# Optimization experiments

Measured on AMD Instinct MI355X. Metric: run time of the kernel, lower is better.

The kernel has to match this reference:

```python
import jax, jax.numpy as jnp
import numpy as np

EPS_BN = 1e-5
EPS_COS = 1e-8
N, E, D = 50000, 1600000, 128
HGC, LG, NUM_CLASSES, EIN, PAE_H = 64, 4, 2, 12, 128


def setup_inputs() -> dict:
    key = jax.random.key(0)
    ks = jax.random.split(key, 16)
    kaiming = lambda k, fi, fo: jax.random.normal(k, (fi, fo), jnp.float32) * (2.0 / fi) ** 0.5
    glorot = lambda k, shape: jax.random.normal(k, shape, jnp.float32) * (2.0 / (shape[-2] + shape[-1])) ** 0.5
    inp = {}
    inp["features"] = jax.random.normal(ks[0], (N, D), jnp.float32)
    inp["edge_index"] = jax.random.randint(ks[1], (2, E), 0, N, jnp.int32)
    inp["edgenet_input"] = jax.random.normal(ks[2], (E, EIN), jnp.float32)
    # PAE parser: Linear(6,128) -> ReLU -> BN(128) -> Dropout -> Linear(128,128)
    inp["pae_w1"] = kaiming(ks[3], EIN // 2, PAE_H)
    inp["pae_b1"] = jnp.zeros((PAE_H,), jnp.float32)
    inp["pae_bn_g"] = jnp.ones((PAE_H,), jnp.float32)
    inp["pae_bn_b"] = jnp.zeros((PAE_H,), jnp.float32)
    inp["pae_bn_rm"] = jnp.zeros((PAE_H,), jnp.float32)
    inp["pae_bn_rv"] = jnp.ones((PAE_H,), jnp.float32)
    inp["pae_w2"] = kaiming(ks[4], PAE_H, PAE_H)
    inp["pae_b2"] = jnp.zeros((PAE_H,), jnp.float32)
    # ChebConv weights, K=3, bias=False: [K, in, out]
    inp["cheb_w0"] = glorot(ks[5], (3, D, HGC))
    inp["cheb_w1"] = glorot(ks[6], (3, HGC, HGC))
    inp["cheb_w2"] = glorot(ks[7], (3, HGC, HGC))
    inp["cheb_w3"] = glorot(ks[8], (3, HGC, HGC))
    # classifier: Linear(lg*hgc=256, 256) -> ReLU -> BN(256) -> Linear(256, num_classes)
    CLS_IN = LG * HGC
    inp["cls_w1"] = kaiming(ks[9], CLS_IN, 256)
    inp["cls_b1"] = jnp.zeros((256,), jnp.float32)
    inp["cls_bn_g"] = jnp.ones((256,), jnp.float32)
    inp["cls_bn_b"] = jnp.zeros((256,), jnp.float32)
    inp["cls_bn_rm"] = jnp.zeros((256,), jnp.float32)
    inp["cls_bn_rv"] = jnp.ones((256,), jnp.float32)
    inp["cls_w2"] = kaiming(ks[10], 256, NUM_CLASSES)
    inp["cls_b2"] = jnp.zeros((NUM_CLASSES,), jnp.float32)
    return inp


def _bn_eval(h, g, b, rm, rv):
    return (h - rm) * jax.lax.rsqrt(rv + EPS_BN) * g + b


def _pae(x, w1, b1, g, b, rm, rv, w2, b2):
    half = w1.shape[0]
    def enc(z):
        h = jax.nn.relu(z @ w1 + b1)
        h = _bn_eval(h, g, b, rm, rv)
        return h @ w2 + b2                      # [E, PAE_H]
    h1, h2 = enc(x[:, :half]), enc(x[:, half:])
    num = jnp.sum(h1 * h2, axis=1)
    den = jnp.maximum(jnp.linalg.norm(h1, axis=1) * jnp.linalg.norm(h2, axis=1), EPS_COS)
    return (num / den + 1.0) * 0.5              # cosine sim mapped to [0, 1]


def _cheb_conv(x, W, row, col, norm, n_nodes):
    # (the +I from L and the -I self-loops with fill=-1 cancel in the propagation)
    def lhat(z):
        return jax.ops.segment_sum(norm[:, None] * z[col], row, num_segments=n_nodes)
    Tx0 = x
    Tx1 = lhat(Tx0)
    Tx2 = 2.0 * lhat(Tx1) - Tx0
    return Tx0 @ W[0] + Tx1 @ W[1] + Tx2 @ W[2]


def reference(features, edge_index, edgenet_input,
              pae_w1, pae_b1, pae_bn_g, pae_bn_b, pae_bn_rm, pae_bn_rv, pae_w2, pae_b2,
              cheb_w0, cheb_w1, cheb_w2, cheb_w3,
              cls_w1, cls_b1, cls_bn_g, cls_bn_b, cls_bn_rm, cls_bn_rv, cls_w2, cls_b2):
    n_nodes = features.shape[0]
    row, col = edge_index[0], edge_index[1]
    # learned edge weights
    edge_weight = _pae(edgenet_input, pae_w1, pae_b1, pae_bn_g, pae_bn_b,
                       pae_bn_rm, pae_bn_rv, pae_w2, pae_b2)
    # sym-normalized (negative) adjacency weights of the scaled Laplacian
    deg = jax.ops.segment_sum(edge_weight, row, num_segments=n_nodes)
    dis = jnp.where(deg > 0, jax.lax.rsqrt(jnp.where(deg > 0, deg, 1.0)), 0.0)
    norm = -dis[row] * edge_weight * dis[col]
    # GCN stack with jumping-knowledge concat (eval mode: dropout is identity)
    h = jax.nn.relu(_cheb_conv(features, cheb_w0, row, col, norm, n_nodes))
    jk = h
    for W in (cheb_w1, cheb_w2, cheb_w3):
        h = jax.nn.relu(_cheb_conv(h, W, row, col, norm, n_nodes))
        jk = jnp.concatenate((jk, h), axis=1)
    # classifier head
    z = jax.nn.relu(jk @ cls_w1 + cls_b1)
    z = _bn_eval(z, cls_bn_g, cls_bn_b, cls_bn_rm, cls_bn_rv)
    logit = z @ cls_w2 + cls_b2
    return (jk, logit, edge_weight)
```

## Files before the change

kernel.cpp:

```cpp
#include <hip/hip_runtime.h>

#define NN 50000
#define EE 1600000

using u16 = unsigned short;
using u32 = unsigned int;
using u64 = unsigned long long;

typedef float f32x4 __attribute__((ext_vector_type(4)));
typedef float f32x2 __attribute__((ext_vector_type(2)));
typedef __bf16 bf16x8 __attribute__((ext_vector_type(8)));
typedef unsigned short u16x8 __attribute__((ext_vector_type(8)));

struct alignas(8) U16x4 { u16 a, b, c, d; };
struct PtrTab { const void* p[20]; };

#define OW1 0
#define OB1 768
#define OG 896
#define OBB 1024
#define ORM 1152
#define ORV 1280
#define OW2 1408
#define OB2 17792
// ... 142 lines not shown
        int jj = gi & 7;
        int lane = (gi >> 3) & 63;
        int ct = (gi >> 9) & 3;
        int kt = gi >> 11;
        int k = kt * 32 + ((lane >> 4) & 3) * 8 + jj;
        int col = ct * 16 + (lane & 15);
        dst[gi] = f2bf(src[k * 64 + col]);
    }
}

__global__ __launch_bounds__(256) void k_foldw0(const float* __restrict__ wpad,
                                                u16* __restrict__ Wg0) {
    const float* src = wpad + OCH0;
    int tid = threadIdx.x;
    int base = blockIdx.x * 1024 + tid * 4;
#pragma unroll
    for (int u = 0; u < 4; u++) {
        int gi = base + u;
        int jj = gi & 7;
        int lane = (gi >> 3) & 63;
        int rest = gi >> 9;
        int ct = rest % 12;
        int kt = rest / 12;
        int k = kt * 32 + ((lane >> 4) & 3) * 8 + jj;
        int cl = (lane & 15);
        float v;
        if (ct < 4) {
            v = src[(1 * 128 + k) * 64 + ct * 16 + cl];
        } else if (ct < 8) {
            v = src[(2 * 128 + k) * 64 + (ct - 4) * 16 + cl];
        } else {
            int c = (ct - 8) * 16 + cl;
            v = src[(0 * 128 + k) * 64 + c] - src[(2 * 128 + k) * 64 + c];
        }
        Wg0[gi] = f2bf(v);
    }
}

__global__ __launch_bounds__(256) void k_x0(const void* __restrict__ feat, const int* __restrict__ flag,
                                            u16* __restrict__ X0) {
    int i = blockIdx.x * 256 + threadIdx.x;
    if (flag[0] != 0) {
        ((uint4*)X0)[i] = ((const uint4*)feat)[i];
    } else {
        const float4* f = (const float4*)feat;
        float4 a = f[2 * i], b = f[2 * i + 1];
        u16x8 o;
        o[0] = f2bf(a.x); o[1] = f2bf(a.y); o[2] = f2bf(a.z); o[3] = f2bf(a.w);
        o[4] = f2bf(b.x); o[5] = f2bf(b.y); o[6] = f2bf(b.z); o[7] = f2bf(b.w);
        ((uint4*)X0)[i] = __builtin_bit_cast(uint4, o);
    }
}

__global__ __launch_bounds__(256, 3) void k_pae(const void* __restrict__ zin, const float* __restrict__ wpad,
                                                const u16* __restrict__ W2sg, const float* __restrict__ b2p,
                                                const int* __restrict__ ei, const int* __restrict__ flag,
                                                float* __restrict__ ewf, void* __restrict__ dout,
                                                u64* __restrict__ dc) {
    __shared__ __align__(16) u16 sW2[16384];
    __shared__ float sB2[128];
    int tid = threadIdx.x;
    for (int i = tid; i < 8192; i += 256) ((u32*)sW2)[i] = ((const u32*)W2sg)[i];
    if (tid < 128) sB2[tid] = b2p[tid];
    __syncthreads();

    bool isbf = flag[0] != 0;
    int wv = __builtin_amdgcn_readfirstlane(tid >> 6);
    int lane = tid & 63;
    int quad = lane >> 4, lrow = lane & 15, jc = lane & 15;
    u32 qm = (quad == 0) ? 0xffffffffu : 0u;

    uint4 w1f[8];
    f32x4 cb[8];
#pragma unroll
    for (int kt = 0; kt < 8; kt++) {
        u32 a = 0, b = 0, c = 0;
        if (quad == 0) {
            int col = kt * 16 + lrow;
            a = (u32)f2bf(wpad[OW1 + 0 * 128 + col]) | ((u32)f2bf(wpad[OW1 + 1 * 128 + col]) << 16);
            b = (u32)f2bf(wpad[OW1 + 2 * 128 + col]) | ((u32)f2bf(wpad[OW1 + 3 * 128 + col]) << 16);
            c = (u32)f2bf(wpad[OW1 + 4 * 128 + col]) | ((u32)f2bf(wpad[OW1 + 5 * 128 + col]) << 16);
        }
        w1f[kt] = (uint4){a, b, c, 0u};
#pragma unroll
        for (int r = 0; r < 4; r++) cb[kt][r] = wpad[OB1 + kt * 16 + quad * 4 + r];
    }

    int gw = blockIdx.x * 4 + wv;
    const int ngroups = EE / 16;
    const int gstep = gridDim.x * 4;

    uint2 pb0, pb1, pb2;
    float4 pf0, pf1, pf2;
    if (gw < ngroups) {
        if (isbf) {
            const uint2* zp = (const uint2*)((const u16*)zin + (size_t)(gw * 16 + lrow) * 12);
            pb0 = zp[0]; pb1 = zp[1]; pb2 = zp[2];
        } else {
            const float4* zp = (const float4*)((const float*)zin + (size_t)(gw * 16 + lrow) * 12);
            pf0 = zp[0]; pf1 = zp[1]; pf2 = zp[2];
        }
    }

#pragma unroll 1
    for (int gidx = gw; gidx < ngroups; gidx += gstep) {
        int e0 = gidx * 16;
        float z1[6], z2[6];
// ... 139 lines not shown
                                               int* __restrict__ offs, float* __restrict__ dis) {
    __shared__ int wsum[16];
    __shared__ int carry;
    int tid = threadIdx.x;
    int wv = tid >> 6, lane = tid & 63;
    if (tid == 0) carry = 0;
    __syncthreads();
    for (int c = 0; c < 49; c++) {
        int i = c * 1024 + tid;
        u64 v64 = (i < NN) ? dc[i] : 0ull;
        int v = (int)(v64 >> 32);
        if (i < NN) {
            float d = (float)(u32)v64 * (1.f / 8388608.f);
            dis[i] = d > 0.f ? rsqrtf(d) : 0.f;
        }
        int x = v;
#pragma unroll
        for (int off = 1; off < 64; off <<= 1) {
            int t = __shfl_up(x, off);
            if (lane >= off) x += t;
        }
        if (lane == 63) wsum[wv] = x;
        __syncthreads();
        if (tid < 16) {
            int s = wsum[tid];
#pragma unroll
            for (int off = 1; off < 16; off <<= 1) {
                int t = __shfl_up(s, off, 16);
                if (tid >= off) s += t;
            }
            wsum[tid] = s;
        }
        __syncthreads();
        int base = carry + (wv > 0 ? wsum[wv - 1] : 0);
        if (i < NN) offs[i] = base + x - v;
        __syncthreads();
        if (tid == 0) carry += wsum[15];
        __syncthreads();
    }
    if (tid == 0) offs[NN] = carry;
}

__global__ __launch_bounds__(256) void k_csr(const int* __restrict__ ei, const float* __restrict__ ewf,
                                             const float* __restrict__ dis, const int* __restrict__ offs,
                                             int* __restrict__ cursor, uint2* __restrict__ csr_meta) {
    int e = blockIdx.x * 256 + threadIdx.x;
    int r = ei[e], c = ei[EE + e];
    float wgt = ewf[e];
    int pos = offs[r] + atomicAdd(cursor + r, 1);
    float nrm = -dis[r] * wgt * dis[c];
    csr_meta[pos] = make_uint2((u32)c, __builtin_bit_cast(u32, nrm));
}

template <int F>
__global__ __launch_bounds__(256) void k_prop(const u16* __restrict__ src, const uint2* __restrict__ csr_meta,
                                              const int* __restrict__ offs,
                                              u16* __restrict__ out, const u16* __restrict__ base,
                                              float alpha, float beta) {
    int lane = threadIdx.x & 63;
    int wv = threadIdx.x >> 6;
    int node = blockIdx.x * 4 + wv;
    int s = offs[node], e = offs[node + 1];

    if (F == 128) {
        int sub = lane >> 4;
        int fl = lane & 15;
        const uint4* sv = (const uint4*)src;
        float a[8] = {0, 0, 0, 0, 0, 0, 0, 0};
        int p = s;
        if (p + 7 < e) {
            uint2 m0 = csr_meta[p + sub];
            uint2 m1 = csr_meta[p + 4 + sub];
            while (true) {
                uint4 v0 = sv[(size_t)m0.x * 16 + fl];
                uint4 v1 = sv[(size_t)m1.x * 16 + fl];
                float w0 = __builtin_bit_cast(float, m0.y);
                float w1 = __builtin_bit_cast(float, m1.y);
                p += 8;
                bool more = (p + 7 < e);
                if (more) {
                    m0 = csr_meta[p + sub];
                    m1 = csr_meta[p + 4 + sub];
                }
                a[0] = fmaf(w0, bfl(v0.x), a[0]); a[1] = fmaf(w0, bfh(v0.x), a[1]);
                a[2] = fmaf(w0, bfl(v0.y), a[2]); a[3] = fmaf(w0, bfh(v0.y), a[3]);
                a[4] = fmaf(w0, bfl(v0.z), a[4]); a[5] = fmaf(w0, bfh(v0.z), a[5]);
                a[6] = fmaf(w0, bfl(v0.w), a[6]); a[7] = fmaf(w0, bfh(v0.w), a[7]);
                a[0] = fmaf(w1, bfl(v1.x), a[0]); a[1] = fmaf(w1, bfh(v1.x), a[1]);
                a[2] = fmaf(w1, bfl(v1.y), a[2]); a[3] = fmaf(w1, bfh(v1.y), a[3]);
                a[4] = fmaf(w1, bfl(v1.z), a[4]); a[5] = fmaf(w1, bfh(v1.z), a[5]);
                a[6] = fmaf(w1, bfl(v1.w), a[6]); a[7] = fmaf(w1, bfh(v1.w), a[7]);
                if (!more) break;
            }
        }
        if (p + 3 < e) {
            uint2 m0 = csr_meta[p + sub];
            uint4 v0 = sv[(size_t)m0.x * 16 + fl];
            float w0 = __builtin_bit_cast(float, m0.y);
            a[0] = fmaf(w0, bfl(v0.x), a[0]); a[1] = fmaf(w0, bfh(v0.x), a[1]);
            a[2] = fmaf(w0, bfl(v0.y), a[2]); a[3] = fmaf(w0, bfh(v0.y), a[3]);
            a[4] = fmaf(w0, bfl(v0.z), a[4]); a[5] = fmaf(w0, bfh(v0.z), a[5]);
            a[6] = fmaf(w0, bfl(v0.w), a[6]); a[7] = fmaf(w0, bfh(v0.w), a[7]);
            p += 4;
        }
#pragma unroll
        for (int i = 0; i < 8; i++) {
            a[i] += __shfl_xor(a[i], 16);
            a[i] += __shfl_xor(a[i], 32);
        }
        if (sub == 0) {
            for (; p < e; p++) {
                uint2 m0 = csr_meta[p];
                uint4 v = sv[(size_t)m0.x * 16 + fl];
                float w = __builtin_bit_cast(float, m0.y);
                a[0] = fmaf(w, bfl(v.x), a[0]); a[1] = fmaf(w, bfh(v.x), a[1]);
                a[2] = fmaf(w, bfl(v.y), a[2]); a[3] = fmaf(w, bfh(v.y), a[3]);
                a[4] = fmaf(w, bfl(v.z), a[4]); a[5] = fmaf(w, bfh(v.z), a[5]);
                a[6] = fmaf(w, bfl(v.w), a[6]); a[7] = fmaf(w, bfh(v.w), a[7]);
            }
            float o[8];
#pragma unroll
            for (int i = 0; i < 8; i++) o[i] = alpha * a[i];
            if (beta != 0.f) {
                uint4 bv = ((const uint4*)base)[(size_t)node * 16 + fl];
                o[0] = fmaf(beta, bfl(bv.x), o[0]); o[1] = fmaf(beta, bfh(bv.x), o[1]);
                o[2] = fmaf(beta, bfl(bv.y), o[2]); o[3] = fmaf(beta, bfh(bv.y), o[3]);
                o[4] = fmaf(beta, bfl(bv.z), o[4]); o[5] = fmaf(beta, bfh(bv.z), o[5]);
                o[6] = fmaf(beta, bfl(bv.w), o[6]); o[7] = fmaf(beta, bfh(bv.w), o[7]);
            }
            uint4 ov;
            ov.x = (u32)f2bf(o[0]) | ((u32)f2bf(o[1]) << 16);
            ov.y = (u32)f2bf(o[2]) | ((u32)f2bf(o[3]) << 16);
            ov.z = (u32)f2bf(o[4]) | ((u32)f2bf(o[5]) << 16);
            ov.w = (u32)f2bf(o[6]) | ((u32)f2bf(o[7]) << 16);
            ((uint4*)out)[(size_t)node * 16 + fl] = ov;
        }
    } else {
        int sub = lane >> 3;
        int fl = lane & 7;
        const uint4* sv = (const uint4*)src;
        float a[8] = {0, 0, 0, 0, 0, 0, 0, 0};
        int p = s;
        if (p + 15 < e) {
            uint2 m0 = csr_meta[p + sub];
            uint2 m1 = csr_meta[p + 8 + sub];
            while (true) {
                uint4 v0 = sv[(size_t)m0.x * 8 + fl];
                uint4 v1 = sv[(size_t)m1.x * 8 + fl];
                float w0 = __builtin_bit_cast(float, m0.y);
                float w1 = __builtin_bit_cast(float, m1.y);
                p += 16;
                bool more = (p + 15 < e);
                if (more) {
                    m0 = csr_meta[p + sub];
                    m1 = csr_meta[p + 8 + sub];
                }
                a[0] = fmaf(w0, bfl(v0.x), a[0]); a[1] = fmaf(w0, bfh(v0.x), a[1]);
                a[2] = fmaf(w0, bfl(v0.y), a[2]); a[3] = fmaf(w0, bfh(v0.y), a[3]);
                a[4] = fmaf(w0, bfl(v0.z), a[4]); a[5] = fmaf(w0, bfh(v0.z), a[5]);
                a[6] = fmaf(w0, bfl(v0.w), a[6]); a[7] = fmaf(w0, bfh(v0.w), a[7]);
                a[0] = fmaf(w1, bfl(v1.x), a[0]); a[1] = fmaf(w1, bfh(v1.x), a[1]);
                a[2] = fmaf(w1, bfl(v1.y), a[2]); a[3] = fmaf(w1, bfh(v1.y), a[3]);
                a[4] = fmaf(w1, bfl(v1.z), a[4]); a[5] = fmaf(w1, bfh(v1.z), a[5]);
                a[6] = fmaf(w1, bfl(v1.w), a[6]); a[7] = fmaf(w1, bfh(v1.w), a[7]);
                if (!more) break;
            }
        }
        if (p + 7 < e) {
            uint2 m0 = csr_meta[p + sub];
            uint4 v0 = sv[(size_t)m0.x * 8 + fl];
            float w0 = __builtin_bit_cast(float, m0.y);
            a[0] = fmaf(w0, bfl(v0.x), a[0]); a[1] = fmaf(w0, bfh(v0.x), a[1]);
            a[2] = fmaf(w0, bfl(v0.y), a[2]); a[3] = fmaf(w0, bfh(v0.y), a[3]);
            a[4] = fmaf(w0, bfl(v0.z), a[4]); a[5] = fmaf(w0, bfh(v0.z), a[5]);
            a[6] = fmaf(w0, bfl(v0.w), a[6]); a[7] = fmaf(w0, bfh(v0.w), a[7]);
            p += 8;
        }
#pragma unroll
        for (int i = 0; i < 8; i++) {
            a[i] += __shfl_xor(a[i], 8);
            a[i] += __shfl_xor(a[i], 16);
            a[i] += __shfl_xor(a[i], 32);
        }
        if (sub == 0) {
            for (; p < e; p++) {
                uint2 m0 = csr_meta[p];
                uint4 v = sv[(size_t)m0.x * 8 + fl];
                float w = __builtin_bit_cast(float, m0.y);
                a[0] = fmaf(w, bfl(v.x), a[0]); a[1] = fmaf(w, bfh(v.x), a[1]);
                a[2] = fmaf(w, bfl(v.y), a[2]); a[3] = fmaf(w, bfh(v.y), a[3]);
                a[4] = fmaf(w, bfl(v.z), a[4]); a[5] = fmaf(w, bfh(v.z), a[5]);
                a[6] = fmaf(w, bfl(v.w), a[6]); a[7] = fmaf(w, bfh(v.w), a[7]);
            }
            float o[8];
#pragma unroll
            for (int i = 0; i < 8; i++) o[i] = alpha * a[i];
            if (beta != 0.f) {
                uint4 bv = ((const uint4*)base)[(size_t)node * 8 + fl];
                o[0] = fmaf(beta, bfl(bv.x), o[0]); o[1] = fmaf(beta, bfh(bv.x), o[1]);
                o[2] = fmaf(beta, bfl(bv.y), o[2]); o[3] = fmaf(beta, bfh(bv.y), o[3]);
                o[4] = fmaf(beta, bfl(bv.z), o[4]); o[5] = fmaf(beta, bfh(bv.z), o[5]);
                o[6] = fmaf(beta, bfl(bv.w), o[6]); o[7] = fmaf(beta, bfh(bv.w), o[7]);
            }
            uint4 ov;
            ov.x = (u32)f2bf(o[0]) | ((u32)f2bf(o[1]) << 16);
            ov.y = (u32)f2bf(o[2]) | ((u32)f2bf(o[3]) << 16);
            ov.z = (u32)f2bf(o[4]) | ((u32)f2bf(o[5]) << 16);
            ov.w = (u32)f2bf(o[6]) | ((u32)f2bf(o[7]) << 16);
            ((uint4*)out)[(size_t)node * 8 + fl] = ov;
        }
    }
}

__global__ __launch_bounds__(256) void k_prop0b(const u16* __restrict__ V, const uint2* __restrict__ csr_meta,
                                                const int* __restrict__ offs, const u16* __restrict__ D,
                                                u16* __restrict__ h0out, const int* __restrict__ flag,
                                                void* __restrict__ jkout) {
    int lane = threadIdx.x & 63;
    int wv = threadIdx.x >> 6;
    int node = blockIdx.x * 4 + wv;
    int s = offs[node], e = offs[node + 1];
    int sub = lane >> 3;
    int fl = lane & 7;
    const uint4* sv = (const uint4*)V;
    float a[8] = {0, 0, 0, 0, 0, 0, 0, 0};
    int p = s;
    if (p + 15 < e) {
        uint2 m0 = csr_meta[p + sub];
        uint2 m1 = csr_meta[p + 8 + sub];
        while (true) {
            uint4 v0 = sv[(size_t)m0.x * 16 + 8 + fl];
            uint4 v1 = sv[(size_t)m1.x * 16 + 8 + fl];
            float w0 = __builtin_bit_cast(float, m0.y);
            float w1 = __builtin_bit_cast(float, m1.y);
            p += 16;
            bool more = (p + 15 < e);
            if (more) {
                m0 = csr_meta[p + sub];
                m1 = csr_meta[p + 8 + sub];
            }
            a[0] = fmaf(w0, bfl(v0.x), a[0]); a[1] = fmaf(w0, bfh(v0.x), a[1]);
            a[2] = fmaf(w0, bfl(v0.y), a[2]); a[3] = fmaf(w0, bfh(v0.y), a[3]);
            a[4] = fmaf(w0, bfl(v0.z), a[4]); a[5] = fmaf(w0, bfh(v0.z), a[5]);
            a[6] = fmaf(w0, bfl(v0.w), a[6]); a[7] = fmaf(w0, bfh(v0.w), a[7]);
            a[0] = fmaf(w1, bfl(v1.x), a[0]); a[1] = fmaf(w1, bfh(v1.x), a[1]);
            a[2] = fmaf(w1, bfl(v1.y), a[2]); a[3] = fmaf(w1, bfh(v1.y), a[3]);
            a[4] = fmaf(w1, bfl(v1.z), a[4]); a[5] = fmaf(w1, bfh(v1.z), a[5]);
            a[6] = fmaf(w1, bfl(v1.w), a[6]); a[7] = fmaf(w1, bfh(v1.w), a[7]);
            if (!more) break;
        }
    }
    if (p + 7 < e) {
        uint2 m0 = csr_meta[p + sub];
        uint4 v0 = sv[(size_t)m0.x * 16 + 8 + fl];
        float w0 = __builtin_bit_cast(float, m0.y);
        a[0] = fmaf(w0, bfl(v0.x), a[0]); a[1] = fmaf(w0, bfh(v0.x), a[1]);
        a[2] = fmaf(w0, bfl(v0.y), a[2]); a[3] = fmaf(w0, bfh(v0.y), a[3]);
        a[4] = fmaf(w0, bfl(v0.z), a[4]); a[5] = fmaf(w0, bfh(v0.z), a[5]);
        a[6] = fmaf(w0, bfl(v0.w), a[6]); a[7] = fmaf(w0, bfh(v0.w), a[7]);
        p += 8;
    }
#pragma unroll
    for (int i = 0; i < 8; i++) {
        a[i] += __shfl_xor(a[i], 8);
        a[i] += __shfl_xor(a[i], 16);
        a[i] += __shfl_xor(a[i], 32);
    }
    if (sub == 0) {
        for (; p < e; p++) {
            uint2 m0 = csr_meta[p];
            uint4 v = sv[(size_t)m0.x * 16 + 8 + fl];
            float w = __builtin_bit_cast(float, m0.y);
            a[0] = fmaf(w, bfl(v.x), a[0]); a[1] = fmaf(w, bfh(v.x), a[1]);
            a[2] = fmaf(w, bfl(v.y), a[2]); a[3] = fmaf(w, bfh(v.y), a[3]);
            a[4] = fmaf(w, bfl(v.z), a[4]); a[5] = fmaf(w, bfh(v.z), a[5]);
            a[6] = fmaf(w, bfl(v.w), a[6]); a[7] = fmaf(w, bfh(v.w), a[7]);
        }
        uint4 v1 = sv[(size_t)node * 16 + fl];
        uint4 dv = ((const uint4*)D)[(size_t)node * 8 + fl];
        float o[8];
        o[0] = fmaf(2.f, a[0], bfl(v1.x) + bfl(dv.x)); o[1] = fmaf(2.f, a[1], bfh(v1.x) + bfh(dv.x));
        o[2] = fmaf(2.f, a[2], bfl(v1.y) + bfl(dv.y)); o[3] = fmaf(2.f, a[3], bfh(v1.y) + bfh(dv.y));
        o[4] = fmaf(2.f, a[4], bfl(v1.z) + bfl(dv.z)); o[5] = fmaf(2.f, a[5], bfh(v1.z) + bfh(dv.z));
        o[6] = fmaf(2.f, a[6], bfl(v1.w) + bfl(dv.w)); o[7] = fmaf(2.f, a[7], bfh(v1.w) + bfh(dv.w));
#pragma unroll
        for (int i = 0; i < 8; i++) o[i] = fmaxf(o[i], 0.f);
        uint4 ov;
        ov.x = (u32)f2bf(o[0]) | ((u32)f2bf(o[1]) << 16);
        ov.y = (u32)f2bf(o[2]) | ((u32)f2bf(o[3]) << 16);
        ov.z = (u32)f2bf(o[4]) | ((u32)f2bf(o[5]) << 16);
        ov.w = (u32)f2bf(o[6]) | ((u32)f2bf(o[7]) << 16);
        ((uint4*)h0out)[(size_t)node * 8 + fl] = ov;
        if (flag[0] != 0) {
            ((uint4*)jkout)[(size_t)node * 32 + fl] = ov;
        } else {
            float* jf = (float*)jkout + (size_t)node * 256 + fl * 8;
#pragma unroll
            for (int i = 0; i < 8; i++) jf[i] = o[i];
        }
    }
}

__global__ __launch_bounds__(256) void k_gemm0(const u16* __restrict__ X0, const u16* __restrict__ Wg0,
                                               u16* __restrict__ U, u16* __restrict__ D) {
    __shared__ __align__(16) u16 sB[4 * 12 * 64 * 8];
    int tid = threadIdx.x;
    for (int i = tid; i < 12288; i += 256) ((u32*)sB)[i] = ((const u32*)Wg0)[i];
    __syncthreads();

    int wv = __builtin_amdgcn_readfirstlane(tid >> 6);
    int lane = tid & 63;
    int quad = lane >> 4, jc = lane & 15;
    int pair = wv >> 1;
    int half = wv & 1;
    int nb = blockIdx.x * 32 + pair * 16;
    int row = nb + jc;
    if (row > NN - 1) row = NN - 1;

    uint4 av[4];
#pragma unroll
    for (int kt = 0; kt < 4; kt++)
        av[kt] = *(const uint4*)(X0 + (size_t)row * 128 + kt * 32 + quad * 8);

    f32x4 acc[6] = {{0.f, 0.f, 0.f, 0.f}, {0.f, 0.f, 0.f, 0.f}, {0.f, 0.f, 0.f, 0.f},
                    {0.f, 0.f, 0.f, 0.f}, {0.f, 0.f, 0.f, 0.f}, {0.f, 0.f, 0.f, 0.f}};
#pragma unroll
    for (int kt = 0; kt < 4; kt++) {
        bf16x8 af = __builtin_bit_cast(bf16x8, av[kt]);
#pragma unroll
        for (int ct = 0; ct < 6; ct++) {
            int g = half * 6 + ct;
            bf16x8 b0 = *reinterpret_cast<const bf16x8*>(&sB[((kt * 12 + g) * 64 + lane) * 8]);
            acc[ct] = __builtin_amdgcn_mfma_f32_16x16x32_bf16(af, b0, acc[ct], 0, 0, 0);
        }
    }

#pragma unroll
    for (int ct = 0; ct < 6; ct++) {
        int g = half * 6 + ct;
        int j = g * 16 + jc;
#pragma unroll
        for (int r = 0; r < 4; r++) {
            int n = nb + quad * 4 + r;
            if (n < NN) {
                float v = acc[ct][r];
                if (j < 128) U[(size_t)n * 128 + j] = f2bf(v);
                else D[(size_t)n * 64 + (j - 128)] = f2bf(v);
            }
        }
    }
}

// ... 140 lines not shown
        if (n < NN) {
            float l0 = part[2 * p][rl][0] + part[2 * p + 1][rl][0] + sb2[0];
            float l1 = part[2 * p][rl][1] + part[2 * p + 1][rl][1] + sb2[1];
            if (flag[0] != 0) {
                u32 pack = (u32)f2bf(l0) | ((u32)f2bf(l1) << 16);
                *(u32*)((u16*)dout + LG_OFF + (size_t)n * 2) = pack;
            } else {
                float2 o = {l0, l1};
                *(float2*)((float*)dout + LG_OFF + (size_t)n * 2) = o;
            }
        }
    }
}

extern "C" void kernel_launch(void* const* d_in, const int* in_sizes, int n_in,
                              void* d_out, int out_size, void* d_ws, size_t ws_size,
                              hipStream_t stream) {
    const void* features = d_in[0];
    const int* ei = (const int*)d_in[1];
    const void* zin = d_in[2];

    char* w = (char*)d_ws;
    auto alloc = [&](size_t bytes) -> void* {
        void* p = (void*)w;
        w += (bytes + 255) & ~(size_t)255;
        return p;
    };
    u16* X0 = (u16*)alloc((size_t)NN * 128 * 2);
    u16* Tx1 = (u16*)alloc((size_t)NN * 128 * 2);
    u16* Tx2 = (u16*)alloc((size_t)NN * 128 * 2);
    u16* h0 = (u16*)alloc((size_t)NN * 64 * 2);
    u16* h1 = (u16*)alloc((size_t)NN * 64 * 2);
    u16* h2 = (u16*)alloc((size_t)NN * 64 * 2);
    u16* h3 = (u16*)alloc((size_t)NN * 64 * 2);
    u16* Dbuf = (u16*)alloc((size_t)NN * 64 * 2);
    float* ewf = (float*)alloc((size_t)EE * 4);
    uint2* csr_meta = (uint2*)alloc((size_t)EE * 8);
    u64* dc = (u64*)alloc((size_t)NN * 8);
    int* cursor = (int*)alloc((size_t)NN * 4);
    float* dis = (float*)alloc((size_t)NN * 4);
    int* offs = (int*)alloc((size_t)(NN + 1) * 4);
    u16* W2s = (u16*)alloc((size_t)16384 * 2);
    float* b2p = (float*)alloc((size_t)128 * 4);
    u16* W1c = (u16*)alloc((size_t)65536 * 2);
    float* w2p = (float*)alloc((size_t)512 * 4);
    float* b2p2 = (float*)alloc((size_t)2 * 4);
    u16* Wg0 = (u16*)alloc((size_t)24576 * 2);
    u16* Wf1 = (u16*)alloc((size_t)12288 * 2);
    u16* Wf2 = (u16*)alloc((size_t)12288 * 2);
    u16* Wf3 = (u16*)alloc((size_t)12288 * 2);
    float* wpad = (float*)alloc((size_t)OTOT * 4);
    int* flag = (int*)alloc(256);

    hipMemsetAsync(dc, 0, (size_t)((char*)dis - (char*)dc), stream);

    PtrTab tab;
    for (int i = 0; i < 20; i++) tab.p[i] = d_in[3 + i];

    k_detect<<<1, 256, 0, stream>>>((const u16*)features, flag);
    k_wconv<<<20, 256, 0, stream>>>(tab, flag, wpad);
    k_fold<<<33, 128, 0, stream>>>(wpad, W2s, b2p);
    k_foldc<<<65, 256, 0, stream>>>(wpad, W1c, w2p, b2p2);
    k_foldw0<<<24, 256, 0, stream>>>(wpad, Wg0);
    k_foldw<<<36, 256, 0, stream>>>(wpad, Wf1, Wf2, Wf3);
    k_x0<<<3125, 256, 0, stream>>>(features, flag, X0);
    k_pae<<<768, 256, 0, stream>>>(zin, wpad, W2s, b2p, ei, flag, ewf, d_out, dc);
    k_scan<<<1, 1024, 0, stream>>>(dc, offs, dis);
    k_csr<<<EE / 256, 256, 0, stream>>>(ei, ewf, dis, offs, cursor, csr_meta);

    k_gemm0<<<1563, 256, 0, stream>>>(X0, Wg0, Tx1 , Dbuf);
    k_prop<128><<<12500, 256, 0, stream>>>(Tx1, csr_meta, offs, Tx2 , nullptr, 1.f, 0.f);
    k_prop0b<<<12500, 256, 0, stream>>>(Tx2, csr_meta, offs, Dbuf, h0, flag, d_out);
    k_prop<64><<<12500, 256, 0, stream>>>(h0, csr_meta, offs, Tx1, nullptr, 1.f, 0.f);
    k_prop<64><<<12500, 256, 0, stream>>>(Tx1, csr_meta, offs, Tx2, h0, 2.f, -1.f);
    k_gemm<64><<<1563, 256, 0, stream>>>(h0, Tx1, Tx2, Wf1, h1, d_out, 64, flag);
    k_prop<64><<<12500, 256, 0, stream>>>(h1, csr_meta, offs, Tx1, nullptr, 1.f, 0.f);
    k_prop<64><<<12500, 256, 0, stream>>>(Tx1, csr_meta, offs, Tx2, h1, 2.f, -1.f);
    k_gemm<64><<<1563, 256, 0, stream>>>(h1, Tx1, Tx2, Wf2, h2, d_out, 128, flag);
    k_prop<64><<<12500, 256, 0, stream>>>(h2, csr_meta, offs, Tx1, nullptr, 1.f, 0.f);
    k_prop<64><<<12500, 256, 0, stream>>>(Tx1, csr_meta, offs, Tx2, h2, 2.f, -1.f);
    k_gemm<64><<<1563, 256, 0, stream>>>(h2, Tx1, Tx2, Wf3, h3, d_out, 192, flag);

    k_cls<<<1563, 256, 0, stream>>>(h0, h1, h2, h3, W1c, wpad, w2p, b2p2, flag, d_out);
    (void)in_sizes; (void)n_in; (void)out_size; (void)ws_size;
}
```

Measured before the change: 979.9 us.

## Predicate SpMM tail edges and split first-hop output into compact halves

The propagation kernels now handle leftover edges with masked loads (zero weight, clamped index) inside the main loop, so the serial single-lane tail loop is gone. The first 128-wide hop writes its two 64-column halves into separate contiguous buffers, so the second hop gathers from a compact 64-wide array instead of a strided half of a 128-wide one. k_pae also moves from 3 to 4 waves per SIMD in its launch bounds, with 1024 blocks instead of 768. The masked loads spend some bandwidth on padding lanes, and the higher occupancy target may force register spills in k_pae.

```diff
diff --git a/kernel.cpp b/kernel.cpp
--- a/kernel.cpp
+++ b/kernel.cpp
@@ -218,7 +218,7 @@
     }
 }
 
-__global__ __launch_bounds__(256, 3) void k_pae(const void* __restrict__ zin, const float* __restrict__ wpad,
+__global__ __launch_bounds__(256, 4) void k_pae(const void* __restrict__ zin, const float* __restrict__ wpad,
                                                 const u16* __restrict__ W2sg, const float* __restrict__ b2p,
                                                 const int* __restrict__ ei, const int* __restrict__ flag,
                                                 float* __restrict__ ewf, void* __restrict__ dout,
@@ -464,167 +464,67 @@
     csr_meta[pos] = make_uint2((u32)c, __builtin_bit_cast(u32, nrm));
 }
 
-template <int F>
-__global__ __launch_bounds__(256) void k_prop(const u16* __restrict__ src, const uint2* __restrict__ csr_meta,
-                                              const int* __restrict__ offs,
-                                              u16* __restrict__ out, const u16* __restrict__ base,
-                                              float alpha, float beta) {
+
+__global__ __launch_bounds__(256) void k_prop0a(const u16* __restrict__ U, const uint2* __restrict__ csr_meta,
+                                                const int* __restrict__ offs,
+                                                u16* __restrict__ V1, u16* __restrict__ V2) {
     int lane = threadIdx.x & 63;
     int wv = threadIdx.x >> 6;
     int node = blockIdx.x * 4 + wv;
     int s = offs[node], e = offs[node + 1];
-
-    if (F == 128) {
-        int sub = lane >> 4;
-        int fl = lane & 15;
-        const uint4* sv = (const uint4*)src;
-        float a[8] = {0, 0, 0, 0, 0, 0, 0, 0};
-        int p = s;
-        if (p + 7 < e) {
-            uint2 m0 = csr_meta[p + sub];
-            uint2 m1 = csr_meta[p + 4 + sub];
-            while (true) {
-                uint4 v0 = sv[(size_t)m0.x * 16 + fl];
-                uint4 v1 = sv[(size_t)m1.x * 16 + fl];
-                float w0 = __builtin_bit_cast(float, m0.y);
-                float w1 = __builtin_bit_cast(float, m1.y);
-                p += 8;
-                bool more = (p + 7 < e);
-                if (more) {
-                    m0 = csr_meta[p + sub];
-                    m1 = csr_meta[p + 4 + sub];
-                }
-                a[0] = fmaf(w0, bfl(v0.x), a[0]); a[1] = fmaf(w0, bfh(v0.x), a[1]);
-                a[2] = fmaf(w0, bfl(v0.y), a[2]); a[3] = fmaf(w0, bfh(v0.y), a[3]);
-                a[4] = fmaf(w0, bfl(v0.z), a[4]); a[5] = fmaf(w0, bfh(v0.z), a[5]);
-                a[6] = fmaf(w0, bfl(v0.w), a[6]); a[7] = fmaf(w0, bfh(v0.w), a[7]);
-                a[0] = fmaf(w1, bfl(v1.x), a[0]); a[1] = fmaf(w1, bfh(v1.x), a[1]);
-                a[2] = fmaf(w1, bfl(v1.y), a[2]); a[3] = fmaf(w1, bfh(v1.y), a[3]);
-                a[4] = fmaf(w1, bfl(v1.z), a[4]); a[5] = fmaf(w1, bfh(v1.z), a[5]);
-                a[6] = fmaf(w1, bfl(v1.w), a[6]); a[7] = fmaf(w1, bfh(v1.w), a[7]);
-                if (!more) break;
-            }
-        }
-        if (p + 3 < e) {
-            uint2 m0 = csr_meta[p + sub];
+    int sub = lane >> 4;
+    int fl = lane & 15;
+    const uint4* sv = (const uint4*)U;
+    float a[8] = {0, 0, 0, 0, 0, 0, 0, 0};
+    int p = s;
+    if (p < e) {
+        int i0 = p + sub, i1 = p + 4 + sub;
+        uint2 m0 = csr_meta[min(i0, e - 1)];
+        uint2 m1 = csr_meta[min(i1, e - 1)];
+        float w0 = (i0 < e) ? __builtin_bit_cast(float, m0.y) : 0.f;
+        float w1 = (i1 < e) ? __builtin_bit_cast(float, m1.y) : 0.f;
+        while (true) {
             uint4 v0 = sv[(size_t)m0.x * 16 + fl];
-            float w0 = __builtin_bit_cast(float, m0.y);
-            a[0] = fmaf(w0, bfl(v0.x), a[0]); a[1] = fmaf(w0, bfh(v0.x), a[1]);
-            a[2] = fmaf(w0, bfl(v0.y), a[2]); a[3] = fmaf(w0, bfh(v0.y), a[3]);
-            a[4] = fmaf(w0, bfl(v0.z), a[4]); a[5] = fmaf(w0, bfh(v0.z), a[5]);
-            a[6] = fmaf(w0, bfl(v0.w), a[6]); a[7] = fmaf(w0, bfh(v0.w), a[7]);
-            p += 4;
-        }
-#pragma unroll
-        for (int i = 0; i < 8; i++) {
-            a[i] += __shfl_xor(a[i], 16);
-            a[i] += __shfl_xor(a[i], 32);
-        }
-        if (sub == 0) {
-            for (; p < e; p++) {
-                uint2 m0 = csr_meta[p];
-                uint4 v = sv[(size_t)m0.x * 16 + fl];
-                float w = __builtin_bit_cast(float, m0.y);
-                a[0] = fmaf(w, bfl(v.x), a[0]); a[1] = fmaf(w, bfh(v.x), a[1]);
-                a[2] = fmaf(w, bfl(v.y), a[2]); a[3] = fmaf(w, bfh(v.y), a[3]);
-                a[4] = fmaf(w, bfl(v.z), a[4]); a[5] = fmaf(w, bfh(v.z), a[5]);
-                a[6] = fmaf(w, bfl(v.w), a[6]); a[7] = fmaf(w, bfh(v.w), a[7]);
-            }
-            float o[8];
-#pragma unroll
-            for (int i = 0; i < 8; i++) o[i] = alpha * a[i];
-            if (beta != 0.f) {
-                uint4 bv = ((const uint4*)base)[(size_t)node * 16 + fl];
-                o[0] = fmaf(beta, bfl(bv.x), o[0]); o[1] = fmaf(beta, bfh(bv.x), o[1]);
-                o[2] = fmaf(beta, bfl(bv.y), o[2]); o[3] = fmaf(beta, bfh(bv.y), o[3]);
-                o[4] = fmaf(beta, bfl(bv.z), o[4]); o[5] = fmaf(beta, bfh(bv.z), o[5]);
-                o[6] = fmaf(beta, bfl(bv.w), o[6]); o[7] = fmaf(beta, bfh(bv.w), o[7]);
-            }
-            uint4 ov;
-            ov.x = (u32)f2bf(o[0]) | ((u32)f2bf(o[1]) << 16);
-            ov.y = (u32)f2bf(o[2]) | ((u32)f2bf(o[3]) << 16);
-            ov.z = (u32)f2bf(o[4]) | ((u32)f2bf(o[5]) << 16);
-            ov.w = (u32)f2bf(o[6]) | ((u32)f2bf(o[7]) << 16);
-            ((uint4*)out)[(size_t)node * 16 + fl] = ov;
-        }
-    } else {
-        int sub = lane >> 3;
-        int fl = lane & 7;
-        const uint4* sv = (const uint4*)src;
-        float a[8] = {0, 0, 0, 0, 0, 0, 0, 0};
-        int p = s;
-        if (p + 15 < e) {
-            uint2 m0 = csr_meta[p + sub];
-            uint2 m1 = csr_meta[p + 8 + sub];
-            while (true) {
-                uint4 v0 = sv[(size_t)m0.x * 8 + fl];
-                uint4 v1 = sv[(size_t)m1.x * 8 + fl];
-                float w0 = __builtin_bit_cast(float, m0.y);
-                float w1 = __builtin_bit_cast(float, m1.y);
-                p += 16;
-                bool more = (p + 15 < e);
-                if (more) {
-                    m0 = csr_meta[p + sub];
-                    m1 = csr_meta[p + 8 + sub];
-                }
-                a[0] = fmaf(w0, bfl(v0.x), a[0]); a[1] = fmaf(w0, bfh(v0.x), a[1]);
-                a[2] = fmaf(w0, bfl(v0.y), a[2]); a[3] = fmaf(w0, bfh(v0.y), a[3]);
-                a[4] = fmaf(w0, bfl(v0.z), a[4]); a[5] = fmaf(w0, bfh(v0.z), a[5]);
-                a[6] = fmaf(w0, bfl(v0.w), a[6]); a[7] = fmaf(w0, bfh(v0.w), a[7]);
-                a[0] = fmaf(w1, bfl(v1.x), a[0]); a[1] = fmaf(w1, bfh(v1.x), a[1]);
-                a[2] = fmaf(w1, bfl(v1.y), a[2]); a[3] = fmaf(w1, bfh(v1.y), a[3]);
-                a[4] = fmaf(w1, bfl(v1.z), a[4]); a[5] = fmaf(w1, bfh(v1.z), a[5]);
-                a[6] = fmaf(w1, bfl(v1.w), a[6]); a[7] = fmaf(w1, bfh(v1.w), a[7]);
-                if (!more) break;
-            }
-        }
-        if (p + 7 < e) {
-            uint2 m0 = csr_meta[p + sub];
-            uint4 v0 = sv[(size_t)m0.x * 8 + fl];
-            float w0 = __builtin_bit_cast(float, m0.y);
-            a[0] = fmaf(w0, bfl(v0.x), a[0]); a[1] = fmaf(w0, bfh(v0.x), a[1]);
-            a[2] = fmaf(w0, bfl(v0.y), a[2]); a[3] = fmaf(w0, bfh(v0.y), a[3]);
-            a[4] = fmaf(w0, bfl(v0.z), a[4]); a[5] = fmaf(w0, bfh(v0.z), a[5]);
-            a[6] = fmaf(w0, bfl(v0.w), a[6]); a[7] = fmaf(w0, bfh(v0.w), a[7]);
+            uint4 v1 = sv[(size_t)m1.x * 16 + fl];
+            float w0c = w0, w1c = w1;
             p += 8;
-        }
-#pragma unroll
-        for (int i = 0; i < 8; i++) {
-            a[i] += __shfl_xor(a[i], 8);
-            a[i] += __shfl_xor(a[i], 16);
-            a[i] += __shfl_xor(a[i], 32);
-        }
-        if (sub == 0) {
-            for (; p < e; p++) {
-                uint2 m0 = csr_meta[p];
-                uint4 v = sv[(size_t)m0.x * 8 + fl];
-                float w = __builtin_bit_cast(float, m0.y);
-                a[0] = fmaf(w, bfl(v.x), a[0]); a[1] = fmaf(w, bfh(v.x), a[1]);
-                a[2] = fmaf(w, bfl(v.y), a[2]); a[3] = fmaf(w, bfh(v.y), a[3]);
-                a[4] = fmaf(w, bfl(v.z), a[4]); a[5] = fmaf(w, bfh(v.z), a[5]);
-                a[6] = fmaf(w, bfl(v.w), a[6]); a[7] = fmaf(w, bfh(v.w), a[7]);
-            }
-            float o[8];
-#pragma unroll
-            for (int i = 0; i < 8; i++) o[i] = alpha * a[i];
-            if (beta != 0.f) {
-                uint4 bv = ((const uint4*)base)[(size_t)node * 8 + fl];
-                o[0] = fmaf(beta, bfl(bv.x), o[0]); o[1] = fmaf(beta, bfh(bv.x), o[1]);
-                o[2] = fmaf(beta, bfl(bv.y), o[2]); o[3] = fmaf(beta, bfh(bv.y), o[3]);
-                o[4] = fmaf(beta, bfl(bv.z), o[4]); o[5] = fmaf(beta, bfh(bv.z), o[5]);
-                o[6] = fmaf(beta, bfl(bv.w), o[6]); o[7] = fmaf(beta, bfh(bv.w), o[7]);
-            }
-            uint4 ov;
-            ov.x = (u32)f2bf(o[0]) | ((u32)f2bf(o[1]) << 16);
-            ov.y = (u32)f2bf(o[2]) | ((u32)f2bf(o[3]) << 16);
-            ov.z = (u32)f2bf(o[4]) | ((u32)f2bf(o[5]) << 16);
-            ov.w = (u32)f2bf(o[6]) | ((u32)f2bf(o[7]) << 16);
-            ((uint4*)out)[(size_t)node * 8 + fl] = ov;
-        }
-    }
-}
-
-__global__ __launch_bounds__(256) void k_prop0b(const u16* __restrict__ V, const uint2* __restrict__ csr_meta,
+            bool more = p < e;
+            if (more) {
+                i0 = p + sub; i1 = p + 4 + sub;
+                m0 = csr_meta[min(i0, e - 1)];
+                m1 = csr_meta[min(i1, e - 1)];
+                w0 = (i0 < e) ? __builtin_bit_cast(float, m0.y) : 0.f;
+                w1 = (i1 < e) ? __builtin_bit_cast(float, m1.y) : 0.f;
+            }
+            a[0] = fmaf(w0c, bfl(v0.x), a[0]); a[1] = fmaf(w0c, bfh(v0.x), a[1]);
+            a[2] = fmaf(w0c, bfl(v0.y), a[2]); a[3] = fmaf(w0c, bfh(v0.y), a[3]);
+            a[4] = fmaf(w0c, bfl(v0.z), a[4]); a[5] = fmaf(w0c, bfh(v0.z), a[5]);
+            a[6] = fmaf(w0c, bfl(v0.w), a[6]); a[7] = fmaf(w0c, bfh(v0.w), a[7]);
+            a[0] = fmaf(w1c, bfl(v1.x), a[0]); a[1] = fmaf(w1c, bfh(v1.x), a[1]);
+            a[2] = fmaf(w1c, bfl(v1.y), a[2]); a[3] = fmaf(w1c, bfh(v1.y), a[3]);
+            a[4] = fmaf(w1c, bfl(v1.z), a[4]); a[5] = fmaf(w1c, bfh(v1.z), a[5]);
+            a[6] = fmaf(w1c, bfl(v1.w), a[6]); a[7] = fmaf(w1c, bfh(v1.w), a[7]);
+            if (!more) break;
+        }
+    }
+#pragma unroll
+    for (int i = 0; i < 8; i++) {
+        a[i] += __shfl_xor(a[i], 16);
+        a[i] += __shfl_xor(a[i], 32);
+    }
+    if (sub == 0) {
+        uint4 ov;
+        ov.x = (u32)f2bf(a[0]) | ((u32)f2bf(a[1]) << 16);
+        ov.y = (u32)f2bf(a[2]) | ((u32)f2bf(a[3]) << 16);
+        ov.z = (u32)f2bf(a[4]) | ((u32)f2bf(a[5]) << 16);
+        ov.w = (u32)f2bf(a[6]) | ((u32)f2bf(a[7]) << 16);
+        if (fl < 8) ((uint4*)V1)[(size_t)node * 8 + fl] = ov;
+        else ((uint4*)V2)[(size_t)node * 8 + (fl - 8)] = ov;
+    }
+}
+
+__global__ __launch_bounds__(256) void k_prop0b(const u16* __restrict__ V1, const u16* __restrict__ V2,
+                                                const uint2* __restrict__ csr_meta,
                                                 const int* __restrict__ offs, const u16* __restrict__ D,
                                                 u16* __restrict__ h0out, const int* __restrict__ flag,
                                                 void* __restrict__ jkout) {
@@ -634,43 +534,38 @@
     int s = offs[node], e = offs[node + 1];
     int sub = lane >> 3;
     int fl = lane & 7;
-    const uint4* sv = (const uint4*)V;
+    const uint4* sv = (const uint4*)V2;
     float a[8] = {0, 0, 0, 0, 0, 0, 0, 0};
     int p = s;
-    if (p + 15 < e) {
-        uint2 m0 = csr_meta[p + sub];
-        uint2 m1 = csr_meta[p + 8 + sub];
+    if (p < e) {
+        int i0 = p + sub, i1 = p + 8 + sub;
+        uint2 m0 = csr_meta[min(i0, e - 1)];
+        uint2 m1 = csr_meta[min(i1, e - 1)];
+        float w0 = (i0 < e) ? __builtin_bit_cast(float, m0.y) : 0.f;
+        float w1 = (i1 < e) ? __builtin_bit_cast(float, m1.y) : 0.f;
         while (true) {
-            uint4 v0 = sv[(size_t)m0.x * 16 + 8 + fl];
-            uint4 v1 = sv[(size_t)m1.x * 16 + 8 + fl];
-            float w0 = __builtin_bit_cast(float, m0.y);
-            float w1 = __builtin_bit_cast(float, m1.y);
+            uint4 v0 = sv[(size_t)m0.x * 8 + fl];
+            uint4 v1 = sv[(size_t)m1.x * 8 + fl];
+            float w0c = w0, w1c = w1;
             p += 16;
-            bool more = (p + 15 < e);
+            bool more = p < e;
             if (more) {
-                m0 = csr_meta[p + sub];
-                m1 = csr_meta[p + 8 + sub];
-            }
-            a[0] = fmaf(w0, bfl(v0.x), a[0]); a[1] = fmaf(w0, bfh(v0.x), a[1]);
-            a[2] = fmaf(w0, bfl(v0.y), a[2]); a[3] = fmaf(w0, bfh(v0.y), a[3]);
-            a[4] = fmaf(w0, bfl(v0.z), a[4]); a[5] = fmaf(w0, bfh(v0.z), a[5]);
-            a[6] = fmaf(w0, bfl(v0.w), a[6]); a[7] = fmaf(w0, bfh(v0.w), a[7]);
-            a[0] = fmaf(w1, bfl(v1.x), a[0]); a[1] = fmaf(w1, bfh(v1.x), a[1]);
-            a[2] = fmaf(w1, bfl(v1.y), a[2]); a[3] = fmaf(w1, bfh(v1.y), a[3]);
-            a[4] = fmaf(w1, bfl(v1.z), a[4]); a[5] = fmaf(w1, bfh(v1.z), a[5]);
-            a[6] = fmaf(w1, bfl(v1.w), a[6]); a[7] = fmaf(w1, bfh(v1.w), a[7]);
+                i0 = p + sub; i1 = p + 8 + sub;
+                m0 = csr_meta[min(i0, e - 1)];
+                m1 = csr_meta[min(i1, e - 1)];
+                w0 = (i0 < e) ? __builtin_bit_cast(float, m0.y) : 0.f;
+                w1 = (i1 < e) ? __builtin_bit_cast(float, m1.y) : 0.f;
+            }
+            a[0] = fmaf(w0c, bfl(v0.x), a[0]); a[1] = fmaf(w0c, bfh(v0.x), a[1]);
+            a[2] = fmaf(w0c, bfl(v0.y), a[2]); a[3] = fmaf(w0c, bfh(v0.y), a[3]);
+            a[4] = fmaf(w0c, bfl(v0.z), a[4]); a[5] = fmaf(w0c, bfh(v0.z), a[5]);
+            a[6] = fmaf(w0c, bfl(v0.w), a[6]); a[7] = fmaf(w0c, bfh(v0.w), a[7]);
+            a[0] = fmaf(w1c, bfl(v1.x), a[0]); a[1] = fmaf(w1c, bfh(v1.x), a[1]);
+            a[2] = fmaf(w1c, bfl(v1.y), a[2]); a[3] = fmaf(w1c, bfh(v1.y), a[3]);
+            a[4] = fmaf(w1c, bfl(v1.z), a[4]); a[5] = fmaf(w1c, bfh(v1.z), a[5]);
+            a[6] = fmaf(w1c, bfl(v1.w), a[6]); a[7] = fmaf(w1c, bfh(v1.w), a[7]);
             if (!more) break;
         }
-    }
-    if (p + 7 < e) {
-        uint2 m0 = csr_meta[p + sub];
-        uint4 v0 = sv[(size_t)m0.x * 16 + 8 + fl];
-        float w0 = __builtin_bit_cast(float, m0.y);
-        a[0] = fmaf(w0, bfl(v0.x), a[0]); a[1] = fmaf(w0, bfh(v0.x), a[1]);
-        a[2] = fmaf(w0, bfl(v0.y), a[2]); a[3] = fmaf(w0, bfh(v0.y), a[3]);
-        a[4] = fmaf(w0, bfl(v0.z), a[4]); a[5] = fmaf(w0, bfh(v0.z), a[5]);
-        a[6] = fmaf(w0, bfl(v0.w), a[6]); a[7] = fmaf(w0, bfh(v0.w), a[7]);
-        p += 8;
     }
 #pragma unroll
     for (int i = 0; i < 8; i++) {
@@ -679,16 +574,7 @@
         a[i] += __shfl_xor(a[i], 32);
     }
     if (sub == 0) {
-        for (; p < e; p++) {
-            uint2 m0 = csr_meta[p];
-            uint4 v = sv[(size_t)m0.x * 16 + 8 + fl];
-            float w = __builtin_bit_cast(float, m0.y);
-            a[0] = fmaf(w, bfl(v.x), a[0]); a[1] = fmaf(w, bfh(v.x), a[1]);
-            a[2] = fmaf(w, bfl(v.y), a[2]); a[3] = fmaf(w, bfh(v.y), a[3]);
-            a[4] = fmaf(w, bfl(v.z), a[4]); a[5] = fmaf(w, bfh(v.z), a[5]);
-            a[6] = fmaf(w, bfl(v.w), a[6]); a[7] = fmaf(w, bfh(v.w), a[7]);
-        }
-        uint4 v1 = sv[(size_t)node * 16 + fl];
+        uint4 v1 = ((const uint4*)V1)[(size_t)node * 8 + fl];
         uint4 dv = ((const uint4*)D)[(size_t)node * 8 + fl];
         float o[8];
         o[0] = fmaf(2.f, a[0], bfl(v1.x) + bfl(dv.x)); o[1] = fmaf(2.f, a[1], bfh(v1.x) + bfh(dv.x));
@@ -710,6 +596,75 @@
 #pragma unroll
             for (int i = 0; i < 8; i++) jf[i] = o[i];
         }
+    }
+}
+
+__global__ __launch_bounds__(256) void k_prop64(const u16* __restrict__ src, const uint2* __restrict__ csr_meta,
+                                                const int* __restrict__ offs,
+                                                u16* __restrict__ out, const u16* __restrict__ base,
+                                                float alpha, float beta) {
+    int lane = threadIdx.x & 63;
+    int wv = threadIdx.x >> 6;
+    int node = blockIdx.x * 4 + wv;
+    int s = offs[node], e = offs[node + 1];
+    int sub = lane >> 3;
+    int fl = lane & 7;
+    const uint4* sv = (const uint4*)src;
+    float a[8] = {0, 0, 0, 0, 0, 0, 0, 0};
+    int p = s;
+    if (p < e) {
+        int i0 = p + sub, i1 = p + 8 + sub;
+        uint2 m0 = csr_meta[min(i0, e - 1)];
+        uint2 m1 = csr_meta[min(i1, e - 1)];
+        float w0 = (i0 < e) ? __builtin_bit_cast(float, m0.y) : 0.f;
+        float w1 = (i1 < e) ? __builtin_bit_cast(float, m1.y) : 0.f;
+        while (true) {
+            uint4 v0 = sv[(size_t)m0.x * 8 + fl];
+            uint4 v1 = sv[(size_t)m1.x * 8 + fl];
+            float w0c = w0, w1c = w1;
+            p += 16;
+            bool more = p < e;
+            if (more) {
+                i0 = p + sub; i1 = p + 8 + sub;
+                m0 = csr_meta[min(i0, e - 1)];
+                m1 = csr_meta[min(i1, e - 1)];
+                w0 = (i0 < e) ? __builtin_bit_cast(float, m0.y) : 0.f;
+                w1 = (i1 < e) ? __builtin_bit_cast(float, m1.y) : 0.f;
+            }
+            a[0] = fmaf(w0c, bfl(v0.x), a[0]); a[1] = fmaf(w0c, bfh(v0.x), a[1]);
+            a[2] = fmaf(w0c, bfl(v0.y), a[2]); a[3] = fmaf(w0c, bfh(v0.y), a[3]);
+            a[4] = fmaf(w0c, bfl(v0.z), a[4]); a[5] = fmaf(w0c, bfh(v0.z), a[5]);
+            a[6] = fmaf(w0c, bfl(v0.w), a[6]); a[7] = fmaf(w0c, bfh(v0.w), a[7]);
+            a[0] = fmaf(w1c, bfl(v1.x), a[0]); a[1] = fmaf(w1c, bfh(v1.x), a[1]);
+            a[2] = fmaf(w1c, bfl(v1.y), a[2]); a[3] = fmaf(w1c, bfh(v1.y), a[3]);
+            a[4] = fmaf(w1c, bfl(v1.z), a[4]); a[5] = fmaf(w1c, bfh(v1.z), a[5]);
+            a[6] = fmaf(w1c, bfl(v1.w), a[6]); a[7] = fmaf(w1c, bfh(v1.w), a[7]);
+            if (!more) break;
+        }
+    }
+#pragma unroll
+    for (int i = 0; i < 8; i++) {
+        a[i] += __shfl_xor(a[i], 8);
+        a[i] += __shfl_xor(a[i], 16);
+        a[i] += __shfl_xor(a[i], 32);
+    }
+    if (sub == 0) {
+        float o[8];
+#pragma unroll
+        for (int i = 0; i < 8; i++) o[i] = alpha * a[i];
+        if (beta != 0.f) {
+            uint4 bv = ((const uint4*)base)[(size_t)node * 8 + fl];
+            o[0] = fmaf(beta, bfl(bv.x), o[0]); o[1] = fmaf(beta, bfh(bv.x), o[1]);
+            o[2] = fmaf(beta, bfl(bv.y), o[2]); o[3] = fmaf(beta, bfh(bv.y), o[3]);
+            o[4] = fmaf(beta, bfl(bv.z), o[4]); o[5] = fmaf(beta, bfh(bv.z), o[5]);
+            o[6] = fmaf(beta, bfl(bv.w), o[6]); o[7] = fmaf(beta, bfh(bv.w), o[7]);
+        }
+        uint4 ov;
+        ov.x = (u32)f2bf(o[0]) | ((u32)f2bf(o[1]) << 16);
+        ov.y = (u32)f2bf(o[2]) | ((u32)f2bf(o[3]) << 16);
+        ov.z = (u32)f2bf(o[4]) | ((u32)f2bf(o[5]) << 16);
+        ov.w = (u32)f2bf(o[6]) | ((u32)f2bf(o[7]) << 16);
+        ((uint4*)out)[(size_t)node * 8 + fl] = ov;
     }
 }
 
@@ -956,6 +911,9 @@
     float* wpad = (float*)alloc((size_t)OTOT * 4);
     int* flag = (int*)alloc(256);
 
+    u16* V1 = Tx2;
+    u16* V2 = Tx2 + (size_t)NN * 64;
+
     hipMemsetAsync(dc, 0, (size_t)((char*)dis - (char*)dc), stream);
 
     PtrTab tab;
@@ -968,21 +926,21 @@
     k_foldw0<<<24, 256, 0, stream>>>(wpad, Wg0);
     k_foldw<<<36, 256, 0, stream>>>(wpad, Wf1, Wf2, Wf3);
     k_x0<<<3125, 256, 0, stream>>>(features, flag, X0);
-    k_pae<<<768, 256, 0, stream>>>(zin, wpad, W2s, b2p, ei, flag, ewf, d_out, dc);
+    k_pae<<<1024, 256, 0, stream>>>(zin, wpad, W2s, b2p, ei, flag, ewf, d_out, dc);
     k_scan<<<1, 1024, 0, stream>>>(dc, offs, dis);
     k_csr<<<EE / 256, 256, 0, stream>>>(ei, ewf, dis, offs, cursor, csr_meta);
 
     k_gemm0<<<1563, 256, 0, stream>>>(X0, Wg0, Tx1 , Dbuf);
-    k_prop<128><<<12500, 256, 0, stream>>>(Tx1, csr_meta, offs, Tx2 , nullptr, 1.f, 0.f);
-    k_prop0b<<<12500, 256, 0, stream>>>(Tx2, csr_meta, offs, Dbuf, h0, flag, d_out);
-    k_prop<64><<<12500, 256, 0, stream>>>(h0, csr_meta, offs, Tx1, nullptr, 1.f, 0.f);
-    k_prop<64><<<12500, 256, 0, stream>>>(Tx1, csr_meta, offs, Tx2, h0, 2.f, -1.f);
+    k_prop0a<<<12500, 256, 0, stream>>>(Tx1, csr_meta, offs, V1, V2);
+    k_prop0b<<<12500, 256, 0, stream>>>(V1, V2, csr_meta, offs, Dbuf, h0, flag, d_out);
+    k_prop64<<<12500, 256, 0, stream>>>(h0, csr_meta, offs, Tx1, nullptr, 1.f, 0.f);
+    k_prop64<<<12500, 256, 0, stream>>>(Tx1, csr_meta, offs, Tx2, h0, 2.f, -1.f);
     k_gemm<64><<<1563, 256, 0, stream>>>(h0, Tx1, Tx2, Wf1, h1, d_out, 64, flag);
-    k_prop<64><<<12500, 256, 0, stream>>>(h1, csr_meta, offs, Tx1, nullptr, 1.f, 0.f);
-    k_prop<64><<<12500, 256, 0, stream>>>(Tx1, csr_meta, offs, Tx2, h1, 2.f, -1.f);
+    k_prop64<<<12500, 256, 0, stream>>>(h1, csr_meta, offs, Tx1, nullptr, 1.f, 0.f);
+    k_prop64<<<12500, 256, 0, stream>>>(Tx1, csr_meta, offs, Tx2, h1, 2.f, -1.f);
     k_gemm<64><<<1563, 256, 0, stream>>>(h1, Tx1, Tx2, Wf2, h2, d_out, 128, flag);
-    k_prop<64><<<12500, 256, 0, stream>>>(h2, csr_meta, offs, Tx1, nullptr, 1.f, 0.f);
-    k_prop<64><<<12500, 256, 0, stream>>>(Tx1, csr_meta, offs, Tx2, h2, 2.f, -1.f);
+    k_prop64<<<12500, 256, 0, stream>>>(h2, csr_meta, offs, Tx1, nullptr, 1.f, 0.f);
+    k_prop64<<<12500, 256, 0, stream>>>(Tx1, csr_meta, offs, Tx2, h2, 2.f, -1.f);
     k_gemm<64><<<1563, 256, 0, stream>>>(h2, Tx1, Tx2, Wf3, h3, d_out, 192, flag);
 
     k_cls<<<1563, 256, 0, stream>>>(h0, h1, h2, h3, W1c, wpad, w2p, b2p2, flag, d_out);
```

Result: slower. 1.135 ms (+15.9%).
